# Kernel optimization log

Measured on AMD Instinct MI355X. Metric: run time of the kernel, lower is better.

## Reference

```python
import jax, jax.numpy as jnp
import numpy as np

N, E, B = 16000, 256000, 32
IN, HID, H1, OUT, H2 = 768, 256, 4, 128, 2
LN_EPS = 1e-5


def _gat_layer(x, src, dst, W, a_src, a_dst, b, heads, out, n, concat):
    # x: (n, in), W: (heads*out, in), a_src/a_dst: (heads, out), b: (heads*out,) or (out,)
    h = (x @ W.T).reshape(n, heads, out)                      # (n, H, out)
    alpha_s = (h * a_src).sum(-1)                             # (n, H)
    alpha_d = (h * a_dst).sum(-1)                             # (n, H)
    e = jax.nn.leaky_relu(alpha_s[src] + alpha_d[dst], 0.2)   # (E', H)
    # segment softmax over incoming edges of each dst node
    m = jax.ops.segment_max(e, dst, num_segments=n)           # (n, H)
    ex = jnp.exp(e - m[dst])
    den = jax.ops.segment_sum(ex, dst, num_segments=n)
    alpha = ex / (den[dst] + 1e-16)                           # (E', H)
    msg = h[src] * alpha[..., None]                           # (E', H, out)
    agg = jax.ops.segment_sum(msg, dst, num_segments=n)       # (n, H, out)
    o = agg.reshape(n, heads * out) if concat else agg.mean(axis=1)
    return o + b


def setup_inputs() -> dict:
    key = jax.random.key(0)
    ks = jax.random.split(key, 16)
    x = jax.random.normal(ks[0], (N, IN), dtype=jnp.float32)
    edge_index = jax.random.randint(ks[1], (2, E), 0, N, dtype=jnp.int32)
    batch = jnp.sort(jax.random.randint(ks[2], (N,), 0, B, dtype=jnp.int32))
    s = 0.05
    return {
        "x": x, "edge_index": edge_index, "batch": batch,
        "W1": jax.random.normal(ks[3], (H1 * HID, IN), jnp.float32) * s,
        "a1_src": jax.random.normal(ks[4], (H1, HID), jnp.float32) * s,
        "a1_dst": jax.random.normal(ks[5], (H1, HID), jnp.float32) * s,
        "b1": jnp.zeros((H1 * HID,), jnp.float32),
        "W2": jax.random.normal(ks[6], (H2 * OUT, H1 * HID), jnp.float32) * s,
        "a2_src": jax.random.normal(ks[7], (H2, OUT), jnp.float32) * s,
        "a2_dst": jax.random.normal(ks[8], (H2, OUT), jnp.float32) * s,
        "b2": jnp.zeros((OUT,), jnp.float32),
        "proj_W": jax.random.normal(ks[9], (768, OUT), jnp.float32) * s,
        "proj_b": jnp.zeros((768,), jnp.float32),
        "ln_g": jnp.ones((768,), jnp.float32),
        "ln_b": jnp.zeros((768,), jnp.float32),
    }


def reference(x, edge_index, batch, W1, a1_src, a1_dst, b1,
              W2, a2_src, a2_dst, b2, proj_W, proj_b, ln_g, ln_b):
    # add self-loops (PyG GATConv default add_self_loops=True)
    loop = jnp.arange(N, dtype=edge_index.dtype)
    src = jnp.concatenate([edge_index[0], loop])
    dst = jnp.concatenate([edge_index[1], loop])

    h1 = jax.nn.elu(_gat_layer(x, src, dst, W1, a1_src, a1_dst, b1, H1, HID, N, True))
    # dropout = 0 (eval mode)
    h2 = jax.nn.elu(_gat_layer(h1, src, dst, W2, a2_src, a2_dst, b2, H2, OUT, N, False))

    # global mean pool per graph
    sums = jax.ops.segment_sum(h2, batch, num_segments=B)            # (B, OUT)
    cnt = jax.ops.segment_sum(jnp.ones((N,), h2.dtype), batch, num_segments=B)
    pooled = sums / jnp.maximum(cnt, 1.0)[:, None]

    z = pooled @ proj_W.T + proj_b                                   # (B, 768)
    mu = z.mean(-1, keepdims=True)
    var = ((z - mu) ** 2).mean(-1, keepdims=True)
    graph_embed = (z - mu) / jnp.sqrt(var + LN_EPS) * ln_g + ln_b
    return graph_embed, h2
```

## Files before the change

### kernel.cpp

```cpp
#include <hip/hip_runtime.h>
#include <cstddef>

#define NN   16000
#define NE   256000
#define EP   (NE + NN)
#define BG   32
#define IN_F 768
#define HID  256
#define H1C  4
#define F1   (H1C * HID)
#define OUTF 128
#define H2C  2
#define F2   (H2C * OUTF)

typedef __bf16 bf16x8 __attribute__((ext_vector_type(8)));
typedef float  f32x4  __attribute__((ext_vector_type(4)));
typedef float  f32x2  __attribute__((ext_vector_type(2)));
typedef unsigned short us8 __attribute__((ext_vector_type(8)));
typedef unsigned short us4 __attribute__((ext_vector_type(4)));

static __device__ __forceinline__ float lrelu02(float x) { return x > 0.f ? x : 0.2f * x; }
static __device__ __forceinline__ float eluf(float x)    { return x > 0.f ? x : expm1f(x); }
static __device__ __forceinline__ unsigned short rne_bf16(float f) {
    unsigned u = __float_as_uint(f);
    return (unsigned short)((u + 0x7fffu + ((u >> 16) & 1u)) >> 16);
}
static __device__ __forceinline__ f32x2 cvt2(unsigned int u) {
    f32x2 r;
    r.x = __uint_as_float(u << 16);
    r.y = __uint_as_float(u & 0xffff0000u);
    return r;
}

#define GLDS16(gp, lp) __builtin_amdgcn_global_load_lds(                         \
    (const __attribute__((address_space(1))) void*)(gp),                          \
    (__attribute__((address_space(3))) void*)(lp), 16, 0, 0)

#define NB_X  ((NN * IN_F) / 1024)
#define NB_W1 ((F1 * IN_F) / 1024)
#define NB_W2 ((F2 * F1) / 1024)
#define NB_H  ((EP + 255) / 256)
#define NB_PREP (NB_X + NB_W1 + NB_W2 + NB_H)

static __device__ __forceinline__ void f2b_body(const float* __restrict__ in,
                                                unsigned short* __restrict__ out,
                                                int blk, int t) {
    int i = (blk * 256 + t) * 4;
    float4 v = *(const float4*)&in[i];
    ushort4 o;
    o.x = rne_bf16(v.x); o.y = rne_bf16(v.y); o.z = rne_bf16(v.z); o.w = rne_bf16(v.w);
    *(ushort4*)&out[i] = o;
}

__global__ __launch_bounds__(256) void k_prep(const float* __restrict__ x,
                                              const float* __restrict__ W1,
                                              const float* __restrict__ W2,
                                              unsigned short* __restrict__ xb,
                                              unsigned short* __restrict__ W1b,
                                              unsigned short* __restrict__ W2b,
                                              const int* __restrict__ ei,
                                              int* __restrict__ deg) {
    int b = blockIdx.x, t = threadIdx.x;
    if (b < NB_X) { f2b_body(x, xb, b, t); return; }
    b -= NB_X;
    if (b < NB_W1) { f2b_body(W1, W1b, b, t); return; }
    b -= NB_W1;
    if (b < NB_W2) { f2b_body(W2, W2b, b, t); return; }
    b -= NB_W2;
    int e = b * 256 + t;
    if (e >= EP) return;
    int d = (e < NE) ? ei[NE + e] : (e - NE);
    atomicAdd(&deg[d], 1);
}

__global__ __launch_bounds__(1024) void k_scan(const int* __restrict__ deg,
                                               int* __restrict__ off, int* __restrict__ cursor) {
    __shared__ int sums[1024];
    int t = threadIdx.x;
    const int CH = 16;
    int base = t * CH;
    int s = 0;
    for (int i = 0; i < CH; ++i) { int idx = base + i; if (idx < NN) s += deg[idx]; }
    sums[t] = s;
    __syncthreads();
    for (int ofs = 1; ofs < 1024; ofs <<= 1) {
        int v = 0;
        if (t >= ofs) v = sums[t - ofs];
        __syncthreads();
        sums[t] += v;
        __syncthreads();
    }
    int run = sums[t] - s;
    for (int i = 0; i < CH; ++i) {
        int idx = base + i;
        if (idx < NN) { off[idx] = run; cursor[idx] = run; run += deg[idx]; }
    }
    if (t == 1023) off[NN] = run;
}

template <int KITER, int HSHIFT, int HCNT>
static __device__ __forceinline__ void gemm_body(const unsigned short* __restrict__ A,
                                                 const unsigned short* __restrict__ B,
                                                 unsigned short* __restrict__ C,
                                                 const float* __restrict__ a_s,
                                                 const float* __restrict__ a_d,
                                                 float* __restrict__ as_o,
                                                 float* __restrict__ ad_o,
                                                 int N, int K, int bx, int by,
                                                 unsigned short* As, unsigned short* Bs,
                                                 int t) {
    const int w = t >> 6, lane = t & 63;
    const int m0 = by * 64, n0 = bx * 128;
    const int wm = (w >> 1) * 32, wn = (w & 1) * 64;

    const unsigned short* ga0 = A + (size_t)(m0 + (t >> 2)) * K + (t & 3) * 8;
    const unsigned short* gb0 = B + (size_t)(n0 + (t >> 2)) * K + (t & 3) * 8;
    const unsigned short* gb1 = gb0 + (size_t)64 * K;
    unsigned short* lA0 = &As[(w * 64) * 8];
    unsigned short* lB0 = &Bs[(w * 64) * 8];
    unsigned short* lB1 = &Bs[(w * 64 + 256) * 8];

    f32x4 acc[2][4] = {};

    const bf16x8* pa = (const bf16x8*)As + (wm + (lane & 15)) * 4 + (lane >> 4);
    const bf16x8* pb = (const bf16x8*)Bs + (wn + (lane & 15)) * 4 + (lane >> 4);

    for (int it = 0; it < KITER; ++it) {
        GLDS16(ga0, lA0);
        GLDS16(gb0, lB0); GLDS16(gb1, lB1);
        ga0 += 32; gb0 += 32; gb1 += 32;
        __syncthreads();
        bf16x8 a0 = pa[0], a1 = pa[64];
        bf16x8 b0 = pb[0], b1 = pb[64], b2 = pb[128], b3 = pb[192];
        acc[0][0] = __builtin_amdgcn_mfma_f32_16x16x32_bf16(a0, b0, acc[0][0], 0, 0, 0);
        acc[0][1] = __builtin_amdgcn_mfma_f32_16x16x32_bf16(a0, b1, acc[0][1], 0, 0, 0);
        acc[0][2] = __builtin_amdgcn_mfma_f32_16x16x32_bf16(a0, b2, acc[0][2], 0, 0, 0);
        acc[0][3] = __builtin_amdgcn_mfma_f32_16x16x32_bf16(a0, b3, acc[0][3], 0, 0, 0);
        acc[1][0] = __builtin_amdgcn_mfma_f32_16x16x32_bf16(a1, b0, acc[1][0], 0, 0, 0);
        acc[1][1] = __builtin_amdgcn_mfma_f32_16x16x32_bf16(a1, b1, acc[1][1], 0, 0, 0);
        acc[1][2] = __builtin_amdgcn_mfma_f32_16x16x32_bf16(a1, b2, acc[1][2], 0, 0, 0);
        acc[1][3] = __builtin_amdgcn_mfma_f32_16x16x32_bf16(a1, b3, acc[1][3], 0, 0, 0);
        __syncthreads();
    }
    const int ccol = n0 + wn + (lane & 15);
    const int crow = m0 + wm + (lane >> 4) * 4;
#pragma unroll
    for (int mi = 0; mi < 2; ++mi)
#pragma unroll
        for (int i = 0; i < 4; ++i) {
            unsigned short* cp = C + (size_t)(crow + mi * 16 + i) * N + ccol;
            cp[0]  = rne_bf16(acc[mi][0][i]);
            cp[16] = rne_bf16(acc[mi][1][i]);
            cp[32] = rne_bf16(acc[mi][2][i]);
            cp[48] = rne_bf16(acc[mi][3][i]);
        }
    const int hh = n0 >> HSHIFT;
    float asv[4], adv[4];
#pragma unroll
    for (int bi = 0; bi < 4; ++bi) {
        asv[bi] = a_s[ccol + bi * 16];
        adv[bi] = a_d[ccol + bi * 16];
    }
#pragma unroll
    for (int mi = 0; mi < 2; ++mi)
#pragma unroll
        for (int i = 0; i < 4; ++i) {
            float vs = acc[mi][0][i] * asv[0] + acc[mi][1][i] * asv[1]
                     + acc[mi][2][i] * asv[2] + acc[mi][3][i] * asv[3];
            float vd = acc[mi][0][i] * adv[0] + acc[mi][1][i] * adv[1]
                     + acc[mi][2][i] * adv[2] + acc[mi][3][i] * adv[3];
#pragma unroll
            for (int m = 1; m <= 8; m <<= 1) {
                vs += __shfl_xor(vs, m);
                vd += __shfl_xor(vd, m);
            }
            if ((lane & 15) == 0) {
                int r = crow + mi * 16 + i;
                atomicAdd(&as_o[r * HCNT + hh], vs);
                atomicAdd(&ad_o[r * HCNT + hh], vd);
            }
        }
}

#define G1_BLKS 2048
__global__ __launch_bounds__(256) void k_gemm1(const unsigned short* __restrict__ A,
                                               const unsigned short* __restrict__ B,
                                               unsigned short* __restrict__ C,
                                               const float* __restrict__ a_s,
                                               const float* __restrict__ a_d,
                                               float* __restrict__ as_o,
                                               float* __restrict__ ad_o,
                                               const int* __restrict__ ei,
                                               int* __restrict__ cursor,
                                               int* __restrict__ csr_src,
                                               int* __restrict__ csr_dst) {
    __shared__ __align__(16) unsigned short As[2048];
    __shared__ __align__(16) unsigned short Bs[4096];
    int blk = blockIdx.x, t = threadIdx.x;
    if (blk < G1_BLKS) {
        int by = (blk & 7) + 8 * (blk >> 6);
        int bx = (blk >> 3) & 7;
        if (by < 250)
            gemm_body<24, 8, 4>(A, B, C, a_s, a_d, as_o, ad_o, F1, IN_F, bx, by, As, Bs, t);
        return;
    }
    int e = (blk - G1_BLKS) * 256 + t;
    if (e >= EP) return;
    int s, d;
    if (e < NE) { s = ei[e]; d = ei[NE + e]; } else { s = d = e - NE; }
    int pos = atomicAdd(&cursor[d], 1);
    csr_src[pos] = s;
    csr_dst[pos] = d;
}

__global__ __launch_bounds__(256) void k_gemm2(const unsigned short* __restrict__ A,
                                               const unsigned short* __restrict__ B,
                                               unsigned short* __restrict__ C,
                                               const float* __restrict__ a_s,
                                               const float* __restrict__ a_d,
                                               float* __restrict__ as_o,
                                               float* __restrict__ ad_o) {
    __shared__ __align__(16) unsigned short As[2048];
    __shared__ __align__(16) unsigned short Bs[4096];
    int blk = blockIdx.x, t = threadIdx.x;
    int by = (blk & 7) + 8 * (blk >> 4);
    int bx = (blk >> 3) & 1;
    if (by < 250)
        gemm_body<32, 7, 2>(A, B, C, a_s, a_d, as_o, ad_o, F2, F1, bx, by, As, Bs, t);
}

__global__ __launch_bounds__(256) void k_el1(const int* __restrict__ csr_src,
                                             const int* __restrict__ csr_dst,
                                             const float* __restrict__ as1,
                                             const float* __restrict__ ad1,
                                             unsigned short* __restrict__ el16) {
    int j = blockIdx.x * 256 + threadIdx.x;
    if (j >= EP) return;
    int s = csr_src[j], d = csr_dst[j];
    float4 av = *(const float4*)&as1[s * H1C];
    float4 dv = *(const float4*)&ad1[d * H1C];
    us4 o;
    o[0] = rne_bf16(expf(lrelu02(av.x + dv.x)));
    o[1] = rne_bf16(expf(lrelu02(av.y + dv.y)));
    o[2] = rne_bf16(expf(lrelu02(av.z + dv.z)));
    o[3] = rne_bf16(expf(lrelu02(av.w + dv.w)));
    *(us4*)&el16[(size_t)j * 4] = o;
}

__global__ __launch_bounds__(256) void k_el2(const int* __restrict__ csr_src,
                                             const int* __restrict__ csr_dst,
                                             const float* __restrict__ as2,
                                             const float* __restrict__ ad2,
                                             float* __restrict__ el) {
    int j = blockIdx.x * 256 + threadIdx.x;
    if (j >= EP) return;
    int s = csr_src[j], d = csr_dst[j];
    float2 av = *(const float2*)&as2[s * 2];
    float2 dv = *(const float2*)&ad2[d * 2];
    float2 o;
    o.x = expf(lrelu02(av.x + dv.x));
    o.y = expf(lrelu02(av.y + dv.y));
    *(float2*)&el[(size_t)j * 2] = o;
}

__global__ __launch_bounds__(256) void k_gat1(const unsigned short* __restrict__ hb,
                                              const unsigned short* __restrict__ el16,
                                              const int* __restrict__ off,
                                              const int* __restrict__ csr,
                                              const int* __restrict__ csrd,
                                              const float* __restrict__ b1,
                                              unsigned short* __restrict__ h1b) {
    __shared__ __align__(16) char sbuf[4][8192];
    const int t = threadIdx.x, l = t & 63, w = t >> 6;
    const int s = blockIdx.x & 7;
    const int db = (blockIdx.x >> 3) * 4 + w;
    const int d0 = db * 16;
    const int h = s >> 1;
    const int g = l >> 4, c = l & 15;
    const int u = c >> 1, odd = c & 1;
    const int beg = off[d0], end = off[d0 + 16];
    char* buf = sbuf[w];
    const char* rbc = buf + g * 2048 + u * 4 + (odd ? 0 : 32);
    const unsigned sel = odd ? 0x03020706u : 0x05040100u;
    const int gfeat = s * 128 + (l >> 3) * 16 + (l & 1) * 8;
    const int slot_in = (l >> 1) & 3;

    f32x4 acc[8] = {};
    f32x4 dacc = {};
    us8 onesu = {0x3F80, 0x3F80, 0x3F80, 0x3F80, 0x3F80, 0x3F80, 0x3F80, 0x3F80};
    bf16x8 ones = *(bf16x8*)&onesu;

    const int nch = (end - beg + 31) >> 5;
    for (int ch = 0; ch < nch; ++ch) {
        const int eb = beg + ch * 32;
#pragma unroll
        for (int cc = 0; cc < 8; ++cc) {
            int slot = eb + cc * 4 + slot_in;
            int sc = slot < end ? slot : end - 1;
            int src = csr[sc];
            GLDS16(hb + (size_t)src * F1 + gfeat, buf + cc * 1024);
        }
        us8 au;
#pragma unroll
        for (int j = 0; j < 8; ++j) {
            int slot = eb + g * 8 + j;
            int sc = slot < end ? slot : end - 1;
            int dv = csrd[sc];
            unsigned short ev = el16[(size_t)sc * 4 + h];
            au[j] = (slot < end && dv == d0 + c) ? ev : (unsigned short)0;
        }
        bf16x8 af = *(bf16x8*)&au;
        asm volatile("s_waitcnt vmcnt(0)" ::: "memory");
        dacc = __builtin_amdgcn_mfma_f32_16x16x32_bf16(af, ones, dacc, 0, 0, 0);
#pragma unroll
        for (int fb = 0; fb < 8; ++fb) {
            const unsigned* p = (const unsigned*)(rbc + fb * 128);
            unsigned W0 = p[0], W1 = p[16], W2 = p[256], W3 = p[272];
            unsigned X0 = (unsigned)__builtin_amdgcn_mov_dpp((int)W0, 0xB1, 0xF, 0xF, true);
            unsigned X1 = (unsigned)__builtin_amdgcn_mov_dpp((int)W1, 0xB1, 0xF, 0xF, true);
            unsigned X2 = (unsigned)__builtin_amdgcn_mov_dpp((int)W2, 0xB1, 0xF, 0xF, true);
            unsigned X3 = (unsigned)__builtin_amdgcn_mov_dpp((int)W3, 0xB1, 0xF, 0xF, true);
            uint4 qq;
            qq.x = __builtin_amdgcn_perm(W0, X0, sel);
            qq.y = __builtin_amdgcn_perm(W1, X1, sel);
            qq.z = __builtin_amdgcn_perm(W2, X2, sel);
            qq.w = __builtin_amdgcn_perm(W3, X3, sel);
            bf16x8 bfv = *(bf16x8*)&qq;
            acc[fb] = __builtin_amdgcn_mfma_f32_16x16x32_bf16(af, bfv, acc[fb], 0, 0, 0);
        }
        asm volatile("s_waitcnt lgkmcnt(0)" ::: "memory");
    }
    float rdh[4];
#pragma unroll
    for (int i = 0; i < 4; ++i) rdh[i] = 1.f / (dacc[i] + 1e-16f);
#pragma unroll
    for (int fb = 0; fb < 8; ++fb) {
        int f = s * 128 + fb * 16 + c;
        float bias = b1[f];
#pragma unroll
        for (int i = 0; i < 4; ++i) {
            int r = d0 + g * 4 + i;
            float v = eluf(acc[fb][i] * rdh[i] + bias);
            h1b[(size_t)r * F1 + f] = rne_bf16(v);
        }
    }
}

__global__ __launch_bounds__(256) void k_gat2(const unsigned short* __restrict__ h2b,
                                              const float* __restrict__ el,
                                              const int* __restrict__ off,
                                              const int* __restrict__ csr,
                                              const float* __restrict__ b2,
                                              float* __restrict__ out_h2) {
    const int l = threadIdx.x & 63;
    const int d = blockIdx.x * 4 + (threadIdx.x >> 6);
    const int beg = off[d], end = off[d + 1];
    const int c = l & 31, p = l >> 5;
    const int myhead = c >> 4;
    const int hw = p;

    float s0 = 0.f, s1 = 0.f;
    for (int j = beg + l; j < end; j += 64) {
        float2 e = *(const float2*)&el[(size_t)j * 2];
        s0 += e.x; s1 += e.y;
    }
    for (int o = 32; o > 0; o >>= 1) {
        s0 += __shfl_down(s0, o);
        s1 += __shfl_down(s1, o);
    }
    s0 = __shfl(s0, 0); s1 = __shfl(s1, 0);
    float rdhw = 1.f / ((hw ? s1 : s0) + 1e-16f);

    f32x2 acc[4] = {};
    const unsigned int* base = (const unsigned int*)h2b + c * 4;
    for (int cbeg = beg; cbeg < end; cbeg += 32) {
        int cnt = end - cbeg; if (cnt > 32) cnt = 32;
        int idx = cbeg + c;
        int idxc = idx < end ? idx : end - 1;
        int s_sel = csr[idxc];
        float ev = el[(size_t)idxc * 2 + hw];
        float myw = (idx < end) ? ev * rdhw : 0.f;
        for (int jj = 0; jj < cnt; jj += 8) {
            int e0 = jj + p * 4;
            int sa = __shfl(s_sel, e0 + 0);
            int sb = __shfl(s_sel, e0 + 1);
            int sc = __shfl(s_sel, e0 + 2);
            int sd = __shfl(s_sel, e0 + 3);
            float wa = __shfl(myw, (myhead << 5) | (e0 + 0));
            float wb = __shfl(myw, (myhead << 5) | (e0 + 1));
            float wc = __shfl(myw, (myhead << 5) | (e0 + 2));
            float wd = __shfl(myw, (myhead << 5) | (e0 + 3));
            uint4 va = *(const uint4*)(base + (unsigned)sa * (F2 / 2));
            uint4 vb = *(const uint4*)(base + (unsigned)sb * (F2 / 2));
            uint4 vc = *(const uint4*)(base + (unsigned)sc * (F2 / 2));
            uint4 vd = *(const uint4*)(base + (unsigned)sd * (F2 / 2));
            f32x2 wa2 = {wa, wa}, wb2 = {wb, wb}, wc2 = {wc, wc}, wd2 = {wd, wd};
            acc[0] += wa2 * cvt2(va.x); acc[1] += wa2 * cvt2(va.y);
            acc[2] += wa2 * cvt2(va.z); acc[3] += wa2 * cvt2(va.w);
            acc[0] += wb2 * cvt2(vb.x); acc[1] += wb2 * cvt2(vb.y);
            acc[2] += wb2 * cvt2(vb.z); acc[3] += wb2 * cvt2(vb.w);
            acc[0] += wc2 * cvt2(vc.x); acc[1] += wc2 * cvt2(vc.y);
            acc[2] += wc2 * cvt2(vc.z); acc[3] += wc2 * cvt2(vc.w);
            acc[0] += wd2 * cvt2(vd.x); acc[1] += wd2 * cvt2(vd.y);
            acc[2] += wd2 * cvt2(vd.z); acc[3] += wd2 * cvt2(vd.w);
        }
    }
    float af[8] = {acc[0].x, acc[0].y, acc[1].x, acc[1].y,
                   acc[2].x, acc[2].y, acc[3].x, acc[3].y};
#pragma unroll
    for (int i = 0; i < 8; ++i) af[i] += __shfl(af[i], l ^ 32);
    float pt[8];
#pragma unroll
    for (int i = 0; i < 8; ++i) pt[i] = __shfl(af[i], l ^ 16);
    if (l < 16) {
        int f = l * 8;
        float o[8];
#pragma unroll
        for (int i = 0; i < 8; ++i) o[i] = eluf(0.5f * (af[i] + pt[i]) + b2[f + i]);
        *(float4*)&out_h2[(size_t)d * OUTF + f]     = make_float4(o[0], o[1], o[2], o[3]);
        *(float4*)&out_h2[(size_t)d * OUTF + f + 4] = make_float4(o[4], o[5], o[6], o[7]);
    }
}

__global__ __launch_bounds__(1024) void k_proj_ln(const float* __restrict__ h2,
                                                  const int* __restrict__ batch,
                                                  const float* __restrict__ pW,
                                                  const float* __restrict__ pb,
                                                  const float* __restrict__ g,
                                                  const float* __restrict__ be,
                                                  float* __restrict__ out) {
    __shared__ float part[1024];
    __shared__ float ph[OUTF];
    __shared__ float zb[768];
    __shared__ float red[1024];
    __shared__ float s_mu, s_rstd;
    int b = blockIdx.x, t = threadIdx.x;
    int lo = 0, hi = NN;
    while (lo < hi) { int mid = (lo + hi) >> 1; if (batch[mid] < b) lo = mid + 1; else hi = mid; }
    int n0 = lo;
    lo = 0; hi = NN;
    while (lo < hi) { int mid = (lo + hi) >> 1; if (batch[mid] < b + 1) lo = mid + 1; else hi = mid; }
    int n1 = lo;
    {
        int f = t & 127, slot = t >> 7;
        float a = 0.f;
        for (int n = n0 + slot; n < n1; n += 8) a += h2[(size_t)n * OUTF + f];
        part[t] = a;
    }
    __syncthreads();
    if (t < OUTF) {
        float s = 0.f;
#pragma unroll
        for (int k = 0; k < 8; ++k) s += part[k * 128 + t];
        float c = (float)(n1 - n0);
        c = c < 1.f ? 1.f : c;
        ph[t] = s / c;
    }
    __syncthreads();
    if (t < 768) {
        float acc = pb[t];
        for (int k = 0; k < OUTF; k += 4) {
            float4 w = *(const float4*)&pW[(size_t)t * OUTF + k];
            acc += w.x * ph[k] + w.y * ph[k + 1] + w.z * ph[k + 2] + w.w * ph[k + 3];
        }
        zb[t] = acc;
    }
    __syncthreads();
    red[t] = (t < 768) ? zb[t] : 0.f;
    __syncthreads();
    for (int ofs = 512; ofs > 0; ofs >>= 1) {
        if (t < ofs) red[t] += red[t + ofs];
        __syncthreads();
    }
    if (t == 0) s_mu = red[0] / 768.f;
    __syncthreads();
    float mu = s_mu;
    float dv = (t < 768) ? (zb[t] - mu) : 0.f;
    red[t] = dv * dv;
    __syncthreads();
    for (int ofs = 512; ofs > 0; ofs >>= 1) {
        if (t < ofs) red[t] += red[t + ofs];
        __syncthreads();
    }
    if (t == 0) s_rstd = rsqrtf(red[0] / 768.f + 1e-5f);
    __syncthreads();
    float rstd = s_rstd;
    if (t < 768)
        out[(size_t)b * 768 + t] = (zb[t] - mu) * rstd * g[t] + be[t];
}

extern "C" void kernel_launch(void* const* d_in, const int* in_sizes, int n_in,
                              void* d_out, int out_size, void* d_ws, size_t ws_size,
                              hipStream_t stream) {
    const float* x    = (const float*)d_in[0];
    const int*   ei   = (const int*)d_in[1];
    const int*   batch= (const int*)d_in[2];
    const float* W1   = (const float*)d_in[3];
    const float* a1s  = (const float*)d_in[4];
    const float* a1d  = (const float*)d_in[5];
    const float* b1   = (const float*)d_in[6];
    const float* W2   = (const float*)d_in[7];
    const float* a2s  = (const float*)d_in[8];
    const float* a2d  = (const float*)d_in[9];
    const float* b2   = (const float*)d_in[10];
    const float* pW   = (const float*)d_in[11];
    const float* pb   = (const float*)d_in[12];
    const float* lng  = (const float*)d_in[13];
    const float* lnb  = (const float*)d_in[14];

    float* out_ge = (float*)d_out;
    float* out_h2 = (float*)d_out + BG * 768;

    char* w = (char*)d_ws;
    unsigned short* xb   = (unsigned short*)w;  w += (size_t)NN * IN_F * 2;
    unsigned short* W1b  = (unsigned short*)w;  w += (size_t)F1 * IN_F * 2;
    unsigned short* W2b  = (unsigned short*)w;  w += (size_t)F2 * F1 * 2;
    unsigned short* hbufb= (unsigned short*)w;  w += (size_t)NN * F1 * 2;
    unsigned short* h1b  = (unsigned short*)w;  w += (size_t)NN * F1 * 2;
    unsigned short* h2b  = (unsigned short*)w;  w += (size_t)NN * F2 * 2;
    float* as1  = (float*)w;  w += (size_t)NN * H1C * 4;
    float* ad1  = (float*)w;  w += (size_t)NN * H1C * 4;
    float* as2  = (float*)w;  w += (size_t)NN * H2C * 4;
    float* ad2  = (float*)w;  w += (size_t)NN * H2C * 4;
    int* deg    = (int*)w;    w += (size_t)NN * 4;
    int* off    = (int*)w;    w += (size_t)(NN + 4) * 4;
    int* cursor = (int*)w;    w += (size_t)NN * 4;
    int* csr    = (int*)w;    w += (size_t)EP * 4;
    int* csrd   = (int*)w;    w += (size_t)EP * 4;
    unsigned short* el16 = (unsigned short*)w;  w += (size_t)EP * H1C * 2;
    float* el2  = (float*)w;  w += (size_t)EP * H2C * 4;

    hipMemsetAsync(as1, 0, (size_t)NN * (H1C + H1C + H2C + H2C + 1) * 4, stream);

    k_prep<<<NB_PREP, 256, 0, stream>>>(x, W1, W2, xb, W1b, W2b, ei, deg);
    k_scan<<<1, 1024, 0, stream>>>(deg, off, cursor);

    k_gemm1<<<G1_BLKS + NB_H, 256, 0, stream>>>(xb, W1b, hbufb, a1s, a1d, as1, ad1,
                                                ei, cursor, csr, csrd);
    k_el1<<<(EP + 255) / 256, 256, 0, stream>>>(csr, csrd, as1, ad1, el16);
    k_gat1<<<2000, 256, 0, stream>>>(hbufb, el16, off, csr, csrd, b1, h1b);

    k_gemm2<<<512, 256, 0, stream>>>(h1b, W2b, h2b, a2s, a2d, as2, ad2);
    k_el2<<<(EP + 255) / 256, 256, 0, stream>>>(csr, csrd, as2, ad2, el2);
    k_gat2<<<NN / 4, 256, 0, stream>>>(h2b, el2, off, csr, b2, out_h2);

    k_proj_ln<<<BG, 1024, 0, stream>>>(out_h2, batch, pW, pb, lng, lnb, out_ge);
}
```

Measured before the change: 413.7 us.

## Prefetch next edge chunk during MFMA and pad LDS layout in gat1

```diff
diff --git a/kernel.cpp b/kernel.cpp
--- a/kernel.cpp
+++ b/kernel.cpp
@@ -270,7 +270,7 @@
                                               const int* __restrict__ csrd,
                                               const float* __restrict__ b1,
                                               unsigned short* __restrict__ h1b) {
-    __shared__ __align__(16) char sbuf[4][8192];
+    __shared__ __align__(16) char sbuf[4][8384];
     const int t = threadIdx.x, l = t & 63, w = t >> 6;
     const int s = blockIdx.x & 7;
     const int db = (blockIdx.x >> 3) * 4 + w;
@@ -280,10 +280,11 @@
     const int u = c >> 1, odd = c & 1;
     const int beg = off[d0], end = off[d0 + 16];
     char* buf = sbuf[w];
-    const char* rbc = buf + g * 2048 + u * 4 + (odd ? 0 : 32);
+    const char* rbc = buf + g * 2112 + u * 4 + (odd ? 0 : 32);
     const unsigned sel = odd ? 0x03020706u : 0x05040100u;
     const int gfeat = s * 128 + (l >> 3) * 16 + (l & 1) * 8;
     const int slot_in = (l >> 1) & 3;
+    const int lA = l & 31;
 
     f32x4 acc[8] = {};
     f32x4 dacc = {};
@@ -291,27 +292,31 @@
     bf16x8 ones = *(bf16x8*)&onesu;
 
     const int nch = (end - beg + 31) >> 5;
+    int dvl, evl;
+    {
+        int slot = beg + lA;
+        int sc2 = slot < end ? slot : end - 1;
+        dvl = (slot < end) ? csrd[sc2] : -1;
+        evl = (int)el16[(size_t)sc2 * 4 + h];
+    }
+#pragma unroll
+    for (int cc = 0; cc < 8; ++cc) {
+        int slot = beg + cc * 4 + slot_in;
+        int sc2 = slot < end ? slot : end - 1;
+        GLDS16(hb + (size_t)csr[sc2] * F1 + gfeat, buf + cc * 1024 + (cc >> 1) * 64);
+    }
     for (int ch = 0; ch < nch; ++ch) {
-        const int eb = beg + ch * 32;
-#pragma unroll
-        for (int cc = 0; cc < 8; ++cc) {
-            int slot = eb + cc * 4 + slot_in;
-            int sc = slot < end ? slot : end - 1;
-            int src = csr[sc];
-            GLDS16(hb + (size_t)src * F1 + gfeat, buf + cc * 1024);
-        }
+        asm volatile("s_waitcnt vmcnt(8)" ::: "memory");
         us8 au;
 #pragma unroll
         for (int j = 0; j < 8; ++j) {
-            int slot = eb + g * 8 + j;
-            int sc = slot < end ? slot : end - 1;
-            int dv = csrd[sc];
-            unsigned short ev = el16[(size_t)sc * 4 + h];
-            au[j] = (slot < end && dv == d0 + c) ? ev : (unsigned short)0;
+            int dvj = __shfl(dvl, g * 8 + j);
+            int evj = __shfl(evl, g * 8 + j);
+            au[j] = (dvj == d0 + c) ? (unsigned short)evj : (unsigned short)0;
         }
         bf16x8 af = *(bf16x8*)&au;
         asm volatile("s_waitcnt vmcnt(0)" ::: "memory");
-        dacc = __builtin_amdgcn_mfma_f32_16x16x32_bf16(af, ones, dacc, 0, 0, 0);
+        uint4 qq[8];
 #pragma unroll
         for (int fb = 0; fb < 8; ++fb) {
             const unsigned* p = (const unsigned*)(rbc + fb * 128);
@@ -320,15 +325,33 @@
             unsigned X1 = (unsigned)__builtin_amdgcn_mov_dpp((int)W1, 0xB1, 0xF, 0xF, true);
             unsigned X2 = (unsigned)__builtin_amdgcn_mov_dpp((int)W2, 0xB1, 0xF, 0xF, true);
             unsigned X3 = (unsigned)__builtin_amdgcn_mov_dpp((int)W3, 0xB1, 0xF, 0xF, true);
-            uint4 qq;
-            qq.x = __builtin_amdgcn_perm(W0, X0, sel);
-            qq.y = __builtin_amdgcn_perm(W1, X1, sel);
-            qq.z = __builtin_amdgcn_perm(W2, X2, sel);
-            qq.w = __builtin_amdgcn_perm(W3, X3, sel);
-            bf16x8 bfv = *(bf16x8*)&qq;
+            qq[fb].x = __builtin_amdgcn_perm(W0, X0, sel);
+            qq[fb].y = __builtin_amdgcn_perm(W1, X1, sel);
+            qq[fb].z = __builtin_amdgcn_perm(W2, X2, sel);
+            qq[fb].w = __builtin_amdgcn_perm(W3, X3, sel);
+        }
+        asm volatile("s_waitcnt lgkmcnt(0)" ::: "memory");
+        __builtin_amdgcn_sched_barrier(0);
+        if (ch + 1 < nch) {
+            const int ebn = beg + (ch + 1) * 32;
+            int slot = ebn + lA;
+            int sc2 = slot < end ? slot : end - 1;
+            int dv2 = (slot < end) ? csrd[sc2] : -1;
+            int ev2 = (int)el16[(size_t)sc2 * 4 + h];
+#pragma unroll
+            for (int cc = 0; cc < 8; ++cc) {
+                int slot2 = ebn + cc * 4 + slot_in;
+                int sc3 = slot2 < end ? slot2 : end - 1;
+                GLDS16(hb + (size_t)csr[sc3] * F1 + gfeat, buf + cc * 1024 + (cc >> 1) * 64);
+            }
+            dvl = dv2; evl = ev2;
+        }
+        dacc = __builtin_amdgcn_mfma_f32_16x16x32_bf16(af, ones, dacc, 0, 0, 0);
+#pragma unroll
+        for (int fb = 0; fb < 8; ++fb) {
+            bf16x8 bfv = *(bf16x8*)&qq[fb];
             acc[fb] = __builtin_amdgcn_mfma_f32_16x16x32_bf16(af, bfv, acc[fb], 0, 0, 0);
         }
-        asm volatile("s_waitcnt lgkmcnt(0)" ::: "memory");
     }
     float rdh[4];
 #pragma unroll
```

Result: no change. 406.6 us (-1.7%).

## Double-buffer gat1 edge-chunk gathers with prefetch two chunks ahead

Applied to the files above, without the earlier changes.

```diff
diff --git a/kernel.cpp b/kernel.cpp
--- a/kernel.cpp
+++ b/kernel.cpp
@@ -263,27 +263,77 @@
     *(float2*)&el[(size_t)j * 2] = o;
 }
 
-__global__ __launch_bounds__(256) void k_gat1(const unsigned short* __restrict__ hb,
+#define ISSUE1(CH, BUF, DV, EV)                                                   \
+    {   int slot_ = beg + (CH) * 32 + lA;                                         \
+        int sc_ = slot_ < end ? slot_ : end - 1;                                  \
+        DV = (slot_ < end) ? csrd[sc_] : -1;                                      \
+        EV = (int)el16[(size_t)sc_ * 4 + h];                                      \
+        _Pragma("unroll")                                                         \
+        for (int cc = 0; cc < 8; ++cc) {                                          \
+            int slot2_ = beg + (CH) * 32 + cc * 4 + slot_in;                      \
+            int sc3_ = slot2_ < end ? slot2_ : end - 1;                           \
+            GLDS16(hb + (size_t)csr[sc3_] * F1 + gfeat,                           \
+                   (BUF) + cc * 1024 + (cc >> 1) * 64);                           \
+        } }
+
+#define STEP1(CH, BUF, DV, EV)                                                    \
+    {   if ((CH) + 1 < nch) asm volatile("s_waitcnt vmcnt(16)" ::: "memory");     \
+        else                asm volatile("s_waitcnt vmcnt(0)" ::: "memory");      \
+        us8 au;                                                                   \
+        _Pragma("unroll")                                                         \
+        for (int j = 0; j < 8; ++j) {                                             \
+            int dvj = __shfl(DV, g * 8 + j);                                      \
+            int evj = __shfl(EV, g * 8 + j);                                      \
+            au[j] = (dvj == d0 + c) ? (unsigned short)evj : (unsigned short)0;    \
+        }                                                                         \
+        bf16x8 af = *(bf16x8*)&au;                                                \
+        const char* rbc_ = (BUF) + g * 2112 + u * 4 + (odd ? 0 : 32);             \
+        uint4 qq[8];                                                              \
+        _Pragma("unroll")                                                         \
+        for (int fb = 0; fb < 8; ++fb) {                                          \
+            const unsigned* p = (const unsigned*)(rbc_ + fb * 128);               \
+            unsigned W0 = p[0], W1 = p[16], W2 = p[256], W3 = p[272];             \
+            unsigned X0 = (unsigned)__builtin_amdgcn_mov_dpp((int)W0, 0xB1, 0xF, 0xF, true); \
+            unsigned X1 = (unsigned)__builtin_amdgcn_mov_dpp((int)W1, 0xB1, 0xF, 0xF, true); \
+            unsigned X2 = (unsigned)__builtin_amdgcn_mov_dpp((int)W2, 0xB1, 0xF, 0xF, true); \
+            unsigned X3 = (unsigned)__builtin_amdgcn_mov_dpp((int)W3, 0xB1, 0xF, 0xF, true); \
+            qq[fb].x = __builtin_amdgcn_perm(W0, X0, sel);                        \
+            qq[fb].y = __builtin_amdgcn_perm(W1, X1, sel);                        \
+            qq[fb].z = __builtin_amdgcn_perm(W2, X2, sel);                        \
+            qq[fb].w = __builtin_amdgcn_perm(W3, X3, sel);                        \
+        }                                                                         \
+        asm volatile("s_waitcnt lgkmcnt(0)" ::: "memory");                        \
+        __builtin_amdgcn_sched_barrier(0);                                       \
+        if ((CH) + 2 < nch) ISSUE1((CH) + 2, BUF, DV, EV);                        \
+        dacc = __builtin_amdgcn_mfma_f32_16x16x32_bf16(af, ones, dacc, 0, 0, 0);  \
+        _Pragma("unroll")                                                         \
+        for (int fb = 0; fb < 8; ++fb) {                                          \
+            bf16x8 bfv = *(bf16x8*)&qq[fb];                                       \
+            acc[fb] = __builtin_amdgcn_mfma_f32_16x16x32_bf16(af, bfv, acc[fb], 0, 0, 0); \
+        } }
+
+__global__ __launch_bounds__(128) void k_gat1(const unsigned short* __restrict__ hb,
                                               const unsigned short* __restrict__ el16,
                                               const int* __restrict__ off,
                                               const int* __restrict__ csr,
                                               const int* __restrict__ csrd,
                                               const float* __restrict__ b1,
                                               unsigned short* __restrict__ h1b) {
-    __shared__ __align__(16) char sbuf[4][8192];
+    __shared__ __align__(16) char sbuf[2][2][8384];
     const int t = threadIdx.x, l = t & 63, w = t >> 6;
     const int s = blockIdx.x & 7;
-    const int db = (blockIdx.x >> 3) * 4 + w;
+    const int db = (blockIdx.x >> 3) * 2 + w;
     const int d0 = db * 16;
     const int h = s >> 1;
     const int g = l >> 4, c = l & 15;
     const int u = c >> 1, odd = c & 1;
     const int beg = off[d0], end = off[d0 + 16];
-    char* buf = sbuf[w];
-    const char* rbc = buf + g * 2048 + u * 4 + (odd ? 0 : 32);
+    char* buf0 = sbuf[w][0];
+    char* buf1 = sbuf[w][1];
     const unsigned sel = odd ? 0x03020706u : 0x05040100u;
     const int gfeat = s * 128 + (l >> 3) * 16 + (l & 1) * 8;
     const int slot_in = (l >> 1) & 3;
+    const int lA = l & 31;
 
     f32x4 acc[8] = {};
     f32x4 dacc = {};
@@ -291,44 +341,13 @@
     bf16x8 ones = *(bf16x8*)&onesu;
 
     const int nch = (end - beg + 31) >> 5;
-    for (int ch = 0; ch < nch; ++ch) {
-        const int eb = beg + ch * 32;
-#pragma unroll
-        for (int cc = 0; cc < 8; ++cc) {
-            int slot = eb + cc * 4 + slot_in;
-            int sc = slot < end ? slot : end - 1;
-            int src = csr[sc];
-            GLDS16(hb + (size_t)src * F1 + gfeat, buf + cc * 1024);
-        }
-        us8 au;
-#pragma unroll
-        for (int j = 0; j < 8; ++j) {
-            int slot = eb + g * 8 + j;
-            int sc = slot < end ? slot : end - 1;
-            int dv = csrd[sc];
-            unsigned short ev = el16[(size_t)sc * 4 + h];
-            au[j] = (slot < end && dv == d0 + c) ? ev : (unsigned short)0;
-        }
-        bf16x8 af = *(bf16x8*)&au;
-        asm volatile("s_waitcnt vmcnt(0)" ::: "memory");
-        dacc = __builtin_amdgcn_mfma_f32_16x16x32_bf16(af, ones, dacc, 0, 0, 0);
-#pragma unroll
-        for (int fb = 0; fb < 8; ++fb) {
-            const unsigned* p = (const unsigned*)(rbc + fb * 128);
-            unsigned W0 = p[0], W1 = p[16], W2 = p[256], W3 = p[272];
-            unsigned X0 = (unsigned)__builtin_amdgcn_mov_dpp((int)W0, 0xB1, 0xF, 0xF, true);
-            unsigned X1 = (unsigned)__builtin_amdgcn_mov_dpp((int)W1, 0xB1, 0xF, 0xF, true);
-            unsigned X2 = (unsigned)__builtin_amdgcn_mov_dpp((int)W2, 0xB1, 0xF, 0xF, true);
-            unsigned X3 = (unsigned)__builtin_amdgcn_mov_dpp((int)W3, 0xB1, 0xF, 0xF, true);
-            uint4 qq;
-            qq.x = __builtin_amdgcn_perm(W0, X0, sel);
-            qq.y = __builtin_amdgcn_perm(W1, X1, sel);
-            qq.z = __builtin_amdgcn_perm(W2, X2, sel);
-            qq.w = __builtin_amdgcn_perm(W3, X3, sel);
-            bf16x8 bfv = *(bf16x8*)&qq;
-            acc[fb] = __builtin_amdgcn_mfma_f32_16x16x32_bf16(af, bfv, acc[fb], 0, 0, 0);
-        }
-        asm volatile("s_waitcnt lgkmcnt(0)" ::: "memory");
+    int dv0, ev0, dv1 = -1, ev1 = 0;
+    ISSUE1(0, buf0, dv0, ev0);
+    asm volatile("" ::: "memory");
+    if (nch > 1) ISSUE1(1, buf1, dv1, ev1);
+    for (int ch = 0; ch < nch; ch += 2) {
+        STEP1(ch, buf0, dv0, ev0);
+        if (ch + 1 < nch) STEP1(ch + 1, buf1, dv1, ev1);
     }
     float rdh[4];
 #pragma unroll
@@ -538,7 +557,7 @@
     k_gemm1<<<G1_BLKS + NB_H, 256, 0, stream>>>(xb, W1b, hbufb, a1s, a1d, as1, ad1,
                                                 ei, cursor, csr, csrd);
     k_el1<<<(EP + 255) / 256, 256, 0, stream>>>(csr, csrd, as1, ad1, el16);
-    k_gat1<<<2000, 256, 0, stream>>>(hbufb, el16, off, csr, csrd, b1, h1b);
+    k_gat1<<<4000, 128, 0, stream>>>(hbufb, el16, off, csr, csrd, b1, h1b);
 
     k_gemm2<<<512, 256, 0, stream>>>(h1b, W2b, h2b, a2s, a2d, as2, ad2);
     k_el2<<<(EP + 255) / 256, 256, 0, stream>>>(csr, csrd, as2, ad2, el2);
```

Result: faster. 396.4 us (-4.2%).
